# Kernel optimization log

Hardware: AMD Instinct MI355X
Metric: run time of the kernel (lower is better)

Reference implementation:

```python
import jax, jax.numpy as jnp
import numpy as np

HIDDEN = 96
INF = 1e30


def setup_inputs() -> dict:
    key = jax.random.key(0)
    ks = jax.random.split(key, 9)
    B, JX, JM, D_IN, D_MEM = 8, 2048, 2048, 150, 150
    GATED = D_IN + D_MEM  # 300
    inputs = jax.random.normal(ks[0], (B, JX, D_IN), dtype=jnp.float32)
    memory = jax.random.normal(ks[1], (B, JM, D_MEM), dtype=jnp.float32)
    mask = jax.random.randint(ks[2], (B, JM), 0, 2, dtype=jnp.int32)
    s_in = 1.0 / np.sqrt(D_IN)
    s_g = 1.0 / np.sqrt(GATED)
    Wi = jax.random.uniform(ks[3], (D_IN, HIDDEN), jnp.float32, -s_in, s_in)
    bi = jax.random.uniform(ks[4], (HIDDEN,), jnp.float32, -s_in, s_in)
    Wm = jax.random.uniform(ks[5], (D_MEM, HIDDEN), jnp.float32, -s_in, s_in)
    bm = jax.random.uniform(ks[6], (HIDDEN,), jnp.float32, -s_in, s_in)
    Wg = jax.random.uniform(ks[7], (GATED, GATED), jnp.float32, -s_g, s_g)
    bg = jax.random.uniform(ks[8], (GATED,), jnp.float32, -s_g, s_g)
    return {"inputs": inputs, "memory": memory, "mask": mask,
            "Wi": Wi, "bi": bi, "Wm": Wm, "bm": bm, "Wg": Wg, "bg": bg}


def reference(inputs, memory, mask, Wi, bi, Wm, bm, Wg, bg):
    # ReLU projections (inference mode: dropout is identity)
    inputs_ = jax.nn.relu(jnp.einsum('bxd,dh->bxh', inputs, Wi) + bi)  # [B,JX,H]
    memory_ = jax.nn.relu(jnp.einsum('byd,dh->byh', memory, Wm) + bm)  # [B,JM,H]
    # Scaled dot-product scores [B,JX,JM]
    scores = jnp.einsum('bxh,byh->bxy', inputs_, memory_) / jnp.sqrt(
        jnp.asarray(HIDDEN, inputs.dtype))
    # Additive mask: -INF where mask==0 (broadcast over JX)
    maskf = mask.astype(inputs.dtype)[:, None, :]  # [B,1,JM]
    scores = scores - INF * (1.0 - maskf)
    logits = jax.nn.softmax(scores, axis=-1)
    outputs = jnp.einsum('bxy,byd->bxd', logits, memory)  # [B,JX,D_MEM]
    res = jnp.concatenate([inputs, outputs], axis=2)  # [B,JX,GATED]
    gate = jax.nn.sigmoid(jnp.einsum('bxg,gk->bxk', res, Wg) + bg)
    return gate * res
```

## Files before the change

kernel.cpp:

```cpp
#include <hip/hip_runtime.h>

#define BB 8
#define JX 2048
#define JMDIM 2048
#define DID 150
#define HID 96
#define GATED 300
#define NSPLIT 4
#define NROWS (BB * JX)

typedef unsigned short u16;
typedef __attribute__((ext_vector_type(8))) short bh8;
typedef __attribute__((ext_vector_type(4))) float f32x4;

#define SCALE2    (0.14724444f)
#define MASK_NEG2 (-1.4426950e30f)

__device__ inline float b2f(u16 u) {
    union { unsigned int i; float f; } c; c.i = ((unsigned int)u) << 16; return c.f;
}
__device__ inline u16 f2b(float f) {
    unsigned int u = __float_as_uint(f);
    unsigned int r = (u + 0x7fffu + ((u >> 16) & 1u)) >> 16;
    return (u16)r;
}

__global__ void prep_kernel(const float* __restrict__ Wi, const float* __restrict__ Wm,
                            const float* __restrict__ Wg,
                            u16* __restrict__ Wti, u16* __restrict__ Wtm,
                            u16* __restrict__ Wgt) {
    int tid = blockIdx.x * blockDim.x + threadIdx.x;
    int nthr = gridDim.x * blockDim.x;
    for (int e = tid; e < 96 * 168; e += nthr) {
        int h = e / 168, d = e - h * 168;
        Wti[e] = (d < DID) ? f2b(Wi[d * HID + h]) : (u16)0;
        Wtm[e] = (d < DID) ? f2b(Wm[d * HID + h]) : (u16)0;
    }
    for (int e = tid; e < 304 * 328; e += nthr) {
        int k = e / 328, d = e - k * 328;
        Wgt[e] = (k < GATED && d < GATED) ? f2b(Wg[d * GATED + k]) : (u16)0;
    }
}

__global__ __launch_bounds__(256) void proj2_kernel(
    const float* __restrict__ inputs, const float* __restrict__ memory,
    const u16* __restrict__ Wti, const u16* __restrict__ Wtm,
    const float* __restrict__ bi, const float* __restrict__ bm,
    u16* __restrict__ Qp, u16* __restrict__ Kp,
    u16* __restrict__ Xi, u16* __restrict__ Vt) {
    __shared__ __align__(16) u16 Xl[64 * 168];
    __shared__ __align__(16) u16 Wl[96 * 168];
    const float *X, *bias; const u16* Wt; u16* Y;
    if (blockIdx.y == 0) { X = inputs; Wt = Wti; bias = bi; Y = Qp; }
    else                 { X = memory; Wt = Wtm; bias = bm; Y = Kp; }
    int tid = threadIdx.x;
    size_t row0 = (size_t)blockIdx.x * 64;

    const float4* Xv = (const float4*)(X + row0 * DID);
    for (int i = tid; i < 2400; i += 256) {
        float4 v = Xv[i];
        int base = i * 4;
#pragma unroll
        for (int k = 0; k < 4; ++k) {
            int idx = base + k;
            int r = idx / DID, d = idx - r * DID;
            Xl[r * 168 + d] = f2b(((const float*)&v)[k]);
        }
    }
    for (int e = tid; e < 64 * 18; e += 256) {
        int r = e / 18, d = 150 + (e - r * 18);
        Xl[r * 168 + d] = 0;
    }
    for (int i = tid; i < 96 * 21; i += 256) {
        *(bh8*)(Wl + i * 8) = *(const bh8*)(Wt + i * 8);
    }
    __syncthreads();

    if (blockIdx.y == 0) {
        for (int e = tid; e < 64 * 20; e += 256) {
            int r = e / 20, c = e - r * 20;
            *(bh8*)(Xi + (row0 + r) * 160 + c * 8) = *(const bh8*)(Xl + r * 168 + c * 8);
        }
    } else {
        int b = blockIdx.x >> 5, jm0 = (blockIdx.x & 31) * 64;
        for (int e = tid; e < 160 * 64; e += 256) {
            int d = e >> 6, c = e & 63;
            u16 v = (d == DID) ? (u16)0x3F80 : Xl[c * 168 + d];
            Vt[((size_t)b * 160 + d) * JMDIM + jm0 + c] = v;
        }
    }

    int wave = tid >> 6, lane = tid & 63, quad = lane >> 4, l15 = lane & 15;
    bh8 af[5];
#pragma unroll
    for (int kc = 0; kc < 5; ++kc)
        af[kc] = *(const bh8*)(Xl + (wave * 16 + l15) * 168 + kc * 32 + quad * 8);
#pragma unroll
    for (int nt = 0; nt < 6; ++nt) {
        f32x4 acc = {0.f, 0.f, 0.f, 0.f};
#pragma unroll
        for (int kc = 0; kc < 5; ++kc) {
            bh8 bf = *(const bh8*)(Wl + (nt * 16 + l15) * 168 + kc * 32 + quad * 8);
            acc = __builtin_amdgcn_mfma_f32_16x16x32_bf16(af[kc], bf, acc, 0, 0, 0);
        }
        int h = nt * 16 + l15;
        float bv = bias[h];
#pragma unroll
        for (int j = 0; j < 4; ++j) {
            float y = acc[j] + bv;
            y = y > 0.f ? y : 0.f;
            Y[(row0 + wave * 16 + quad * 4 + j) * HID + h] = f2b(y);
        }
    }
}

template <int SPLIT>
__global__ __launch_bounds__(256, 2) void attn_kernel(
    const u16* __restrict__ Qp, const u16* __restrict__ Kp,
    const u16* __restrict__ Vt, const int* __restrict__ mask,
    u16* __restrict__ Opart, float* __restrict__ lpart) {
    __shared__ __align__(16) u16 Kl[64 * 104];
    __shared__ __align__(16) u16 Vl[160 * 72];
    __shared__ __align__(16) u16 Pl[128 * 72];
    __shared__ float Ml[64];
    const int b = blockIdx.y;
    const int x0 = blockIdx.x * 128;
    const int tid = threadIdx.x;
    const int wave = tid >> 6, lane = tid & 63;
    const int quad = lane >> 4, l15 = lane & 15;

    bh8 qf[2][3];
#pragma unroll
    for (int mt = 0; mt < 2; ++mt) {
        const u16* qb = Qp + ((size_t)b * JX + x0 + wave * 32 + mt * 16 + l15) * HID + quad * 8;
        qf[mt][0] = *(const bh8*)(qb);
        qf[mt][1] = *(const bh8*)(qb + 32);
        qf[mt][2] = *(const bh8*)(qb + 64);
    }

    f32x4 o[2][10];
    const f32x4 zero4 = {0.f, 0.f, 0.f, 0.f};
#pragma unroll
    for (int mt = 0; mt < 2; ++mt)
#pragma unroll
        for (int i = 0; i < 10; ++i) o[mt][i] = zero4;

    const int nIter = 32 / SPLIT;
    const int jm0_0 = blockIdx.z * nIter * 64;

    const u16* kptr[3]; u16* kdst[3];
#pragma unroll
    for (int t = 0; t < 3; ++t) {
        int i = tid + t * 256, r = i / 12, c = i - r * 12;
        kptr[t] = Kp + ((size_t)b * JMDIM + jm0_0 + r) * HID + c * 8;
        kdst[t] = Kl + r * 104 + c * 8;
    }
    const u16* vptr[5]; u16* vdst[5];
#pragma unroll
    for (int t = 0; t < 5; ++t) {
        int i = tid + t * 256, d = i >> 3, c = i & 7;
        vptr[t] = Vt + ((size_t)b * 160 + d) * JMDIM + jm0_0 + c * 8;
        vdst[t] = Vl + d * 72 + c * 8;
    }
    const int* mptr = mask + b * JMDIM + jm0_0 + (tid & 63);

    bh8 kreg[3], vreg[5]; int mreg = 0;
#pragma unroll
    for (int t = 0; t < 3; ++t) { kreg[t] = *(const bh8*)kptr[t]; kptr[t] += 64 * HID; }
#pragma unroll
    for (int t = 0; t < 5; ++t) { vreg[t] = *(const bh8*)vptr[t]; vptr[t] += 64; }
    if (tid < 64) { mreg = *mptr; mptr += 64; }

    for (int it = 0; it < nIter; ++it) {
        __syncthreads();
#pragma unroll
        for (int t = 0; t < 3; ++t) *(bh8*)kdst[t] = kreg[t];
#pragma unroll
        for (int t = 0; t < 5; ++t) *(bh8*)vdst[t] = vreg[t];
        if (tid < 64) Ml[tid] = mreg ? 0.f : MASK_NEG2;
        if (it + 1 < nIter) {
#pragma unroll
            for (int t = 0; t < 3; ++t) { kreg[t] = *(const bh8*)kptr[t]; kptr[t] += 64 * HID; }
#pragma unroll
            for (int t = 0; t < 5; ++t) { vreg[t] = *(const bh8*)vptr[t]; vptr[t] += 64; }
            if (tid < 64) { mreg = *mptr; mptr += 64; }
        }
        __syncthreads();

        f32x4 s[2][4];
#pragma unroll
        for (int mt = 0; mt < 2; ++mt)
#pragma unroll
            for (int nt = 0; nt < 4; ++nt) s[mt][nt] = zero4;
#pragma unroll
        for (int nt = 0; nt < 4; ++nt) {
#pragma unroll
            for (int kc = 0; kc < 3; ++kc) {
                bh8 bf = *(const bh8*)(Kl + (nt * 16 + l15) * 104 + kc * 32 + quad * 8);
                s[0][nt] = __builtin_amdgcn_mfma_f32_16x16x32_bf16(qf[0][kc], bf, s[0][nt], 0, 0, 0);
                s[1][nt] = __builtin_amdgcn_mfma_f32_16x16x32_bf16(qf[1][kc], bf, s[1][nt], 0, 0, 0);
            }
        }
#pragma unroll
        for (int nt = 0; nt < 4; ++nt) {
            float madd = Ml[nt * 16 + l15];
#pragma unroll
            for (int mt = 0; mt < 2; ++mt)
#pragma unroll
                for (int j = 0; j < 4; ++j) {
                    float p = exp2f(s[mt][nt][j] * SCALE2 + madd);
                    Pl[(wave * 32 + mt * 16 + quad * 4 + j) * 72 + nt * 16 + l15] = f2b(p);
                }
        }
        __threadfence_block();

        bh8 pf[2][2];
#pragma unroll
        for (int mt = 0; mt < 2; ++mt) {
            pf[mt][0] = *(const bh8*)(Pl + (wave * 32 + mt * 16 + l15) * 72 + quad * 8);
            pf[mt][1] = *(const bh8*)(Pl + (wave * 32 + mt * 16 + l15) * 72 + 32 + quad * 8);
        }
#pragma unroll
        for (int nt = 0; nt < 10; ++nt) {
#pragma unroll
            for (int kc = 0; kc < 2; ++kc) {
                bh8 bf = *(const bh8*)(Vl + (nt * 16 + l15) * 72 + kc * 32 + quad * 8);
                o[0][nt] = __builtin_amdgcn_mfma_f32_16x16x32_bf16(pf[0][kc], bf, o[0][nt], 0, 0, 0);
                o[1][nt] = __builtin_amdgcn_mfma_f32_16x16x32_bf16(pf[1][kc], bf, o[1][nt], 0, 0, 0);
            }
        }
    }

    const size_t z = blockIdx.z;
    const int srcLane = (lane & 48) | 6;
#pragma unroll
    for (int mt = 0; mt < 2; ++mt) {
        float lv[4], inv[4];
#pragma unroll
        for (int j = 0; j < 4; ++j) {
            lv[j] = __shfl(o[mt][9][j], srcLane, 64);
            inv[j] = (lv[j] > 0.f) ? 1.f / lv[j] : 0.f;
        }
        size_t grow = (size_t)b * JX + x0 + wave * 32 + mt * 16;
#pragma unroll
        for (int nt = 0; nt < 10; ++nt) {
            int d = nt * 16 + l15;
            if (d < 152) {
#pragma unroll
                for (int j = 0; j < 4; ++j)
                    Opart[(z * NROWS + grow + quad * 4 + j) * 152 + d] = f2b(o[mt][nt][j] * inv[j]);
            }
        }
        if (l15 == 0) {
#pragma unroll
            for (int j = 0; j < 4; ++j)
                lpart[z * NROWS + grow + quad * 4 + j] = lv[j];
        }
    }
}

template <int SPLIT>
__global__ __launch_bounds__(256) void gate_kernel(
    const u16* __restrict__ Xi, const u16* __restrict__ Opart,
    const float* __restrict__ lpart,
    const u16* __restrict__ Wgt, const float* __restrict__ bg,
    float* __restrict__ out) {
    __shared__ __align__(16) u16 Rl[16 * 328];
    __shared__ float Cw[SPLIT * 16];
    int tid = threadIdx.x;
    size_t row0 = (size_t)blockIdx.x * 16;

    if (tid < 16) {
        float l[SPLIT], L = 0.f;
#pragma unroll
        for (int s = 0; s < SPLIT; ++s) {
            l[s] = lpart[(size_t)s * NROWS + row0 + tid];
            L += l[s];
        }
        float invL = (L > 0.f) ? 1.f / L : 0.f;
#pragma unroll
        for (int s = 0; s < SPLIT; ++s) Cw[s * 16 + tid] = l[s] * invL;
    }
    for (int e = tid; e < 16 * 20; e += 256) {
        int r = e / 20, c = e - r * 20;
        *(bh8*)(Rl + r * 328 + c * 8) = *(const bh8*)(Xi + (row0 + r) * 160 + c * 8);
    }
    __syncthreads();
    for (int e = tid; e < 16 * 19; e += 256) {
        int r = e / 19, q = e - r * 19;
        float acc[8];
#pragma unroll
        for (int k = 0; k < 8; ++k) acc[k] = 0.f;
#pragma unroll
        for (int s = 0; s < SPLIT; ++s) {
            bh8 v = *(const bh8*)(Opart + ((size_t)s * NROWS + row0 + r) * 152 + q * 8);
            float w = Cw[s * 16 + r];
#pragma unroll
            for (int k = 0; k < 8; ++k) acc[k] += b2f(((const u16*)&v)[k]) * w;
        }
        u16* dst = Rl + r * 328 + 150 + q * 8;
#pragma unroll
        for (int k = 0; k < 8; ++k) dst[k] = f2b(acc[k]);
    }
    for (int e = tid; e < 16 * 26; e += 256) {
        int r = e / 26, c = 302 + (e - r * 26);
        Rl[r * 328 + c] = 0;
    }
    __syncthreads();

    int wave = tid >> 6, lane = tid & 63, quad = lane >> 4, l15 = lane & 15;
    bh8 af[10];
#pragma unroll
    for (int kc = 0; kc < 10; ++kc)
        af[kc] = *(const bh8*)(Rl + l15 * 328 + kc * 32 + quad * 8);
    for (int nt = wave; nt < 19; nt += 4) {
        int h = nt * 16 + l15;
        f32x4 acc = {0.f, 0.f, 0.f, 0.f};
#pragma unroll
        for (int kc = 0; kc < 10; ++kc) {
            bh8 bf = *(const bh8*)(Wgt + (size_t)h * 328 + kc * 32 + quad * 8);
            acc = __builtin_amdgcn_mfma_f32_16x16x32_bf16(af[kc], bf, acc, 0, 0, 0);
        }
        if (h < GATED) {
            float bv = bg[h];
#pragma unroll
            for (int j = 0; j < 4; ++j) {
                int r = quad * 4 + j;
                float x = acc[j] + bv;
                float g = 1.f / (1.f + __expf(-x));
                float rv = b2f(Rl[r * 328 + h]);
                out[(row0 + r) * GATED + h] = g * rv;
            }
        }
    }
}

extern "C" void kernel_launch(void* const* d_in, const int* in_sizes, int n_in,
                              void* d_out, int out_size, void* d_ws, size_t ws_size,
                              hipStream_t stream) {
    const float* inputs = (const float*)d_in[0];
    const float* memory = (const float*)d_in[1];
    const int*   mask   = (const int*)d_in[2];
    const float* Wi = (const float*)d_in[3];
    const float* bi = (const float*)d_in[4];
    const float* Wm = (const float*)d_in[5];
    const float* bm = (const float*)d_in[6];
    const float* Wg = (const float*)d_in[7];
    const float* bg = (const float*)d_in[8];
    float* out = (float*)d_out;

    u16* Qp  = (u16*)d_ws;
    u16* Kp  = Qp + (size_t)NROWS * HID;
    u16* Vt  = Kp + (size_t)NROWS * HID;
    u16* Xi  = Vt + (size_t)BB * 160 * JMDIM;
    u16* Wti = Xi + (size_t)NROWS * 160;
    u16* Wtm = Wti + 96 * 168;
    u16* Wgt = Wtm + 96 * 168;
    u16* Opart = Wgt + 304 * 328;
    size_t u16_elems = (size_t)(Opart - Qp) + (size_t)NSPLIT * NROWS * 152;
    size_t base_bytes = ((u16_elems * sizeof(u16)) + 15) & ~(size_t)15;
    float* lpart = (float*)((char*)d_ws + base_bytes);
    size_t needed = base_bytes + (size_t)NSPLIT * NROWS * sizeof(float);
    if (ws_size < needed) return;

    prep_kernel<<<dim3(128), 256, 0, stream>>>(Wi, Wm, Wg, Wti, Wtm, Wgt);
    proj2_kernel<<<dim3(NROWS / 64, 2), 256, 0, stream>>>(
        inputs, memory, Wti, Wtm, bi, bm, Qp, Kp, Xi, Vt);
    attn_kernel<NSPLIT><<<dim3(JX / 128, BB, NSPLIT), 256, 0, stream>>>(
        Qp, Kp, Vt, mask, Opart, lpart);
    gate_kernel<NSPLIT><<<dim3(NROWS / 16), 256, 0, stream>>>(
        Xi, Opart, lpart, Wgt, bg, out);
}
```

Before: 147.6 us.

## Compact unmasked memory rows and skip masked keys in attention

```diff
diff --git a/kernel.cpp b/kernel.cpp
--- a/kernel.cpp
+++ b/kernel.cpp
@@ -14,7 +14,6 @@
 typedef __attribute__((ext_vector_type(4))) float f32x4;
 
 #define SCALE2    (0.14724444f)
-#define MASK_NEG2 (-1.4426950e30f)
 
 __device__ inline float b2f(u16 u) {
     union { unsigned int i; float f; } c; c.i = ((unsigned int)u) << 16; return c.f;
@@ -25,12 +24,38 @@
     return (u16)r;
 }
 
-__global__ void prep_kernel(const float* __restrict__ Wi, const float* __restrict__ Wm,
-                            const float* __restrict__ Wg,
-                            u16* __restrict__ Wti, u16* __restrict__ Wtm,
-                            u16* __restrict__ Wgt) {
-    int tid = blockIdx.x * blockDim.x + threadIdx.x;
-    int nthr = gridDim.x * blockDim.x;
+__global__ __launch_bounds__(256) void prep_kernel(
+    const float* __restrict__ Wi, const float* __restrict__ Wm,
+    const float* __restrict__ Wg, const int* __restrict__ mask,
+    u16* __restrict__ Wti, u16* __restrict__ Wtm, u16* __restrict__ Wgt,
+    int* __restrict__ idx, int* __restrict__ mcount) {
+    if (blockIdx.x >= 128) {
+        __shared__ int wsum[4];
+        int b = blockIdx.x - 128;
+        int tid = threadIdx.x;
+        const int* m = mask + (size_t)b * JMDIM;
+        int v[8], cnt = 0;
+#pragma unroll
+        for (int k = 0; k < 8; ++k) { v[k] = m[tid * 8 + k]; cnt += v[k]; }
+        int lane = tid & 63, wave = tid >> 6;
+        int sc = cnt;
+        for (int off = 1; off < 64; off <<= 1) {
+            int t = __shfl_up(sc, off, 64);
+            if (lane >= off) sc += t;
+        }
+        if (lane == 63) wsum[wave] = sc;
+        __syncthreads();
+        int wbase = 0;
+        for (int w = 0; w < wave; ++w) wbase += wsum[w];
+        int base = wbase + sc - cnt;
+        int* ib = idx + (size_t)b * JMDIM;
+#pragma unroll
+        for (int k = 0; k < 8; ++k) if (v[k]) ib[base++] = tid * 8 + k;
+        if (tid == 255) mcount[b] = base;
+        return;
+    }
+    int tid = blockIdx.x * 256 + threadIdx.x;
+    const int nthr = 128 * 256;
     for (int e = tid; e < 96 * 168; e += nthr) {
         int h = e / 168, d = e - h * 168;
         Wti[e] = (d < DID) ? f2b(Wi[d * HID + h]) : (u16)0;
@@ -42,28 +67,23 @@
     }
 }
 
-__global__ __launch_bounds__(256) void proj2_kernel(
-    const float* __restrict__ inputs, const float* __restrict__ memory,
-    const u16* __restrict__ Wti, const u16* __restrict__ Wtm,
-    const float* __restrict__ bi, const float* __restrict__ bm,
-    u16* __restrict__ Qp, u16* __restrict__ Kp,
-    u16* __restrict__ Xi, u16* __restrict__ Vt) {
+__global__ __launch_bounds__(256) void projq_kernel(
+    const float* __restrict__ inputs, const u16* __restrict__ Wti,
+    const float* __restrict__ bi,
+    u16* __restrict__ Qp, u16* __restrict__ Xi) {
     __shared__ __align__(16) u16 Xl[64 * 168];
     __shared__ __align__(16) u16 Wl[96 * 168];
-    const float *X, *bias; const u16* Wt; u16* Y;
-    if (blockIdx.y == 0) { X = inputs; Wt = Wti; bias = bi; Y = Qp; }
-    else                 { X = memory; Wt = Wtm; bias = bm; Y = Kp; }
     int tid = threadIdx.x;
     size_t row0 = (size_t)blockIdx.x * 64;
 
-    const float4* Xv = (const float4*)(X + row0 * DID);
+    const float4* Xv = (const float4*)(inputs + row0 * DID);
     for (int i = tid; i < 2400; i += 256) {
         float4 v = Xv[i];
         int base = i * 4;
 #pragma unroll
         for (int k = 0; k < 4; ++k) {
-            int idx = base + k;
-            int r = idx / DID, d = idx - r * DID;
+            int id = base + k;
+            int r = id / DID, d = id - r * DID;
             Xl[r * 168 + d] = f2b(((const float*)&v)[k]);
         }
     }
@@ -72,22 +92,13 @@
         Xl[r * 168 + d] = 0;
     }
     for (int i = tid; i < 96 * 21; i += 256) {
-        *(bh8*)(Wl + i * 8) = *(const bh8*)(Wt + i * 8);
+        *(bh8*)(Wl + i * 8) = *(const bh8*)(Wti + i * 8);
     }
     __syncthreads();
 
-    if (blockIdx.y == 0) {
-        for (int e = tid; e < 64 * 20; e += 256) {
-            int r = e / 20, c = e - r * 20;
-            *(bh8*)(Xi + (row0 + r) * 160 + c * 8) = *(const bh8*)(Xl + r * 168 + c * 8);
-        }
-    } else {
-        int b = blockIdx.x >> 5, jm0 = (blockIdx.x & 31) * 64;
-        for (int e = tid; e < 160 * 64; e += 256) {
-            int d = e >> 6, c = e & 63;
-            u16 v = (d == DID) ? (u16)0x3F80 : Xl[c * 168 + d];
-            Vt[((size_t)b * 160 + d) * JMDIM + jm0 + c] = v;
-        }
+    for (int e = tid; e < 64 * 20; e += 256) {
+        int r = e / 20, c = e - r * 20;
+        *(bh8*)(Xi + (row0 + r) * 160 + c * 8) = *(const bh8*)(Xl + r * 168 + c * 8);
     }
 
     int wave = tid >> 6, lane = tid & 63, quad = lane >> 4, l15 = lane & 15;
@@ -104,12 +115,85 @@
             acc = __builtin_amdgcn_mfma_f32_16x16x32_bf16(af[kc], bf, acc, 0, 0, 0);
         }
         int h = nt * 16 + l15;
-        float bv = bias[h];
+        float bv = bi[h];
 #pragma unroll
         for (int j = 0; j < 4; ++j) {
             float y = acc[j] + bv;
             y = y > 0.f ? y : 0.f;
-            Y[(row0 + wave * 16 + quad * 4 + j) * HID + h] = f2b(y);
+            Qp[(row0 + wave * 16 + quad * 4 + j) * HID + h] = f2b(y);
+        }
+    }
+}
+
+__global__ __launch_bounds__(256) void projkv_kernel(
+    const float* __restrict__ memory, const u16* __restrict__ Wtm,
+    const float* __restrict__ bm, const int* __restrict__ idx,
+    const int* __restrict__ mcount,
+    u16* __restrict__ Kp, u16* __restrict__ Vt) {
+    __shared__ __align__(16) u16 Xl[64 * 168];
+    __shared__ __align__(16) u16 Wl[96 * 168];
+    __shared__ int Il[64];
+    const int b = blockIdx.y, s = blockIdx.x;
+    const int mc = mcount[b];
+    const int ntiles = (mc + 63) >> 6;
+    if (s >= ntiles) return;
+    const int tid = threadIdx.x;
+    const int jc0 = s * 64;
+
+    if (tid < 64) {
+        int jc = jc0 + tid;
+        Il[tid] = (jc < mc) ? idx[(size_t)b * JMDIM + jc] : -1;
+    }
+    for (int i = tid; i < 96 * 21; i += 256) {
+        *(bh8*)(Wl + i * 8) = *(const bh8*)(Wtm + i * 8);
+    }
+    __syncthreads();
+
+    const float* Mb = memory + (size_t)b * JMDIM * DID;
+    for (int e = tid; e < 64 * 75; e += 256) {
+        int r = e / 75, c = e - r * 75;
+        int row = Il[r];
+        float2 val = make_float2(0.f, 0.f);
+        if (row >= 0) val = *(const float2*)(Mb + (size_t)row * DID + c * 2);
+        Xl[r * 168 + c * 2]     = f2b(val.x);
+        Xl[r * 168 + c * 2 + 1] = f2b(val.y);
+    }
+    for (int e = tid; e < 64 * 18; e += 256) {
+        int r = e / 18, d = 150 + (e - r * 18);
+        Xl[r * 168 + d] = 0;
+    }
+    __syncthreads();
+
+    for (int e = tid; e < 160 * 64; e += 256) {
+        int d = e >> 6, c = e & 63;
+        int jc = jc0 + c;
+        u16 v;
+        if (d < DID)       v = Xl[c * 168 + d];
+        else if (d == DID) v = (jc < mc) ? (u16)0x3F80 : (u16)0;
+        else               v = 0;
+        Vt[((size_t)b * 160 + d) * JMDIM + jc] = v;
+    }
+
+    int wave = tid >> 6, lane = tid & 63, quad = lane >> 4, l15 = lane & 15;
+    bh8 af[5];
+#pragma unroll
+    for (int kc = 0; kc < 5; ++kc)
+        af[kc] = *(const bh8*)(Xl + (wave * 16 + l15) * 168 + kc * 32 + quad * 8);
+#pragma unroll
+    for (int nt = 0; nt < 6; ++nt) {
+        f32x4 acc = {0.f, 0.f, 0.f, 0.f};
+#pragma unroll
+        for (int kc = 0; kc < 5; ++kc) {
+            bh8 bf = *(const bh8*)(Wl + (nt * 16 + l15) * 168 + kc * 32 + quad * 8);
+            acc = __builtin_amdgcn_mfma_f32_16x16x32_bf16(af[kc], bf, acc, 0, 0, 0);
+        }
+        int h = nt * 16 + l15;
+        float bv = bm[h];
+#pragma unroll
+        for (int j = 0; j < 4; ++j) {
+            float y = acc[j] + bv;
+            y = y > 0.f ? y : 0.f;
+            Kp[((size_t)b * JMDIM + jc0 + wave * 16 + quad * 4 + j) * HID + h] = f2b(y);
         }
     }
 }
@@ -117,18 +201,22 @@
 template <int SPLIT>
 __global__ __launch_bounds__(256, 2) void attn_kernel(
     const u16* __restrict__ Qp, const u16* __restrict__ Kp,
-    const u16* __restrict__ Vt, const int* __restrict__ mask,
+    const u16* __restrict__ Vt, const int* __restrict__ mcount,
     u16* __restrict__ Opart, float* __restrict__ lpart) {
     __shared__ __align__(16) u16 Kl[64 * 104];
     __shared__ __align__(16) u16 Vl[160 * 72];
     __shared__ __align__(16) u16 Pl[128 * 72];
-    __shared__ float Ml[64];
     const int b = blockIdx.y;
     const int x0 = blockIdx.x * 128;
     const int tid = threadIdx.x;
     const int wave = tid >> 6, lane = tid & 63;
     const int quad = lane >> 4, l15 = lane & 15;
 
+    const int mc = mcount[b];
+    const int ntiles = (mc + 63) >> 6;
+    const int zi = blockIdx.z;
+    const int myT = (ntiles > zi) ? ((ntiles - 1 - zi) / SPLIT + 1) : 0;
+
     bh8 qf[2][3];
 #pragma unroll
     for (int mt = 0; mt < 2; ++mt) {
@@ -145,8 +233,7 @@
 #pragma unroll
         for (int i = 0; i < 10; ++i) o[mt][i] = zero4;
 
-    const int nIter = 32 / SPLIT;
-    const int jm0_0 = blockIdx.z * nIter * 64;
+    const int jm0_0 = zi * 64;
 
     const u16* kptr[3]; u16* kdst[3];
 #pragma unroll
@@ -162,28 +249,26 @@
         vptr[t] = Vt + ((size_t)b * 160 + d) * JMDIM + jm0_0 + c * 8;
         vdst[t] = Vl + d * 72 + c * 8;
     }
-    const int* mptr = mask + b * JMDIM + jm0_0 + (tid & 63);
-
-    bh8 kreg[3], vreg[5]; int mreg = 0;
-#pragma unroll
-    for (int t = 0; t < 3; ++t) { kreg[t] = *(const bh8*)kptr[t]; kptr[t] += 64 * HID; }
-#pragma unroll
-    for (int t = 0; t < 5; ++t) { vreg[t] = *(const bh8*)vptr[t]; vptr[t] += 64; }
-    if (tid < 64) { mreg = *mptr; mptr += 64; }
-
-    for (int it = 0; it < nIter; ++it) {
+
+    bh8 kreg[3], vreg[5];
+    if (myT > 0) {
+#pragma unroll
+        for (int t = 0; t < 3; ++t) { kreg[t] = *(const bh8*)kptr[t]; kptr[t] += SPLIT * 64 * HID; }
+#pragma unroll
+        for (int t = 0; t < 5; ++t) { vreg[t] = *(const bh8*)vptr[t]; vptr[t] += SPLIT * 64; }
+    }
+
+    for (int it = 0; it < myT; ++it) {
         __syncthreads();
 #pragma unroll
         for (int t = 0; t < 3; ++t) *(bh8*)kdst[t] = kreg[t];
 #pragma unroll
         for (int t = 0; t < 5; ++t) *(bh8*)vdst[t] = vreg[t];
-        if (tid < 64) Ml[tid] = mreg ? 0.f : MASK_NEG2;
-        if (it + 1 < nIter) {
-#pragma unroll
-            for (int t = 0; t < 3; ++t) { kreg[t] = *(const bh8*)kptr[t]; kptr[t] += 64 * HID; }
-#pragma unroll
-            for (int t = 0; t < 5; ++t) { vreg[t] = *(const bh8*)vptr[t]; vptr[t] += 64; }
-            if (tid < 64) { mreg = *mptr; mptr += 64; }
+        if (it + 1 < myT) {
+#pragma unroll
+            for (int t = 0; t < 3; ++t) { kreg[t] = *(const bh8*)kptr[t]; kptr[t] += SPLIT * 64 * HID; }
+#pragma unroll
+            for (int t = 0; t < 5; ++t) { vreg[t] = *(const bh8*)vptr[t]; vptr[t] += SPLIT * 64; }
         }
         __syncthreads();
 
@@ -203,12 +288,11 @@
         }
 #pragma unroll
         for (int nt = 0; nt < 4; ++nt) {
-            float madd = Ml[nt * 16 + l15];
 #pragma unroll
             for (int mt = 0; mt < 2; ++mt)
 #pragma unroll
                 for (int j = 0; j < 4; ++j) {
-                    float p = exp2f(s[mt][nt][j] * SCALE2 + madd);
+                    float p = exp2f(s[mt][nt][j] * SCALE2);
                     Pl[(wave * 32 + mt * 16 + quad * 4 + j) * 72 + nt * 16 + l15] = f2b(p);
                 }
         }
@@ -360,14 +444,19 @@
     size_t u16_elems = (size_t)(Opart - Qp) + (size_t)NSPLIT * NROWS * 152;
     size_t base_bytes = ((u16_elems * sizeof(u16)) + 15) & ~(size_t)15;
     float* lpart = (float*)((char*)d_ws + base_bytes);
-    size_t needed = base_bytes + (size_t)NSPLIT * NROWS * sizeof(float);
+    int* idx = (int*)(lpart + (size_t)NSPLIT * NROWS);
+    int* mcountp = idx + (size_t)BB * JMDIM;
+    size_t needed = base_bytes + (size_t)NSPLIT * NROWS * sizeof(float)
+                  + (size_t)BB * JMDIM * sizeof(int) + BB * sizeof(int);
     if (ws_size < needed) return;
 
-    prep_kernel<<<dim3(128), 256, 0, stream>>>(Wi, Wm, Wg, Wti, Wtm, Wgt);
-    proj2_kernel<<<dim3(NROWS / 64, 2), 256, 0, stream>>>(
-        inputs, memory, Wti, Wtm, bi, bm, Qp, Kp, Xi, Vt);
+    prep_kernel<<<dim3(136), 256, 0, stream>>>(Wi, Wm, Wg, mask, Wti, Wtm, Wgt,
+                                               idx, mcountp);
+    projq_kernel<<<dim3(NROWS / 64), 256, 0, stream>>>(inputs, Wti, bi, Qp, Xi);
+    projkv_kernel<<<dim3(32, BB), 256, 0, stream>>>(memory, Wtm, bm, idx, mcountp,
+                                                    Kp, Vt);
     attn_kernel<NSPLIT><<<dim3(JX / 128, BB, NSPLIT), 256, 0, stream>>>(
-        Qp, Kp, Vt, mask, Opart, lpart);
+        Qp, Kp, Vt, mcountp, Opart, lpart);
     gate_kernel<NSPLIT><<<dim3(NROWS / 16), 256, 0, stream>>>(
         Xi, Opart, lpart, Wgt, bg, out);
 }
```

New measurement: 147.8 us. No clear change (+0.1%).
